# Kernel optimization log

Measured on AMD Instinct MI355X. Metric: run time of the kernel, lower is better.

## Reference

```python
import jax, jax.numpy as jnp
import numpy as np

B, S, H, DH = 2, 4096, 8, 64
D = H * DH


def setup_inputs() -> dict:
    key = jax.random.key(0)
    ks = jax.random.split(key, 6)
    std = 1.0 / np.sqrt(D)
    return {
        "x": jax.random.normal(ks[0], (B, S, D), dtype=jnp.float32),
        "Wq": jax.random.normal(ks[1], (D, D), dtype=jnp.float32) * std,
        "Wk": jax.random.normal(ks[2], (D, D), dtype=jnp.float32) * std,
        "Wv": jax.random.normal(ks[3], (D, D), dtype=jnp.float32) * std,
        "Wo": jax.random.normal(ks[4], (D, D), dtype=jnp.float32) * std,
        "bo": jnp.zeros((D,), dtype=jnp.float32),
    }


def reference(x, Wq, Wk, Wv, Wo, bo):
    scale = DH ** (-0.5)
    # torch Linear: y = x @ W.T
    q = x @ Wq.T  # [B,S,D]
    k = x @ Wk.T
    v = x @ Wv.T
    # split heads -> [B,H,S,Dh]
    q = q.reshape(B, S, H, DH).transpose(0, 2, 1, 3)
    k = k.reshape(B, S, H, DH).transpose(0, 2, 1, 3)
    v = v.reshape(B, S, H, DH).transpose(0, 2, 1, 3)
    score = jnp.einsum('bhqd,bhkd->bhqk', q, k) * scale  # [B,H,S,S]
    weights = jax.nn.softmax(score, axis=-1)
    attn = jnp.einsum('bhqk,bhkd->bhqd', weights, v)  # [B,H,S,Dh]
    h_ = attn.transpose(0, 2, 1, 3).reshape(B, S, D)
    return h_ @ Wo.T + bo
```

## Files before the change

kernel.cpp:

```cpp
#include <hip/hip_runtime.h>

#define LOG2E 1.44269504088896340736f

typedef unsigned short u16;
typedef __bf16 bf16x4_t __attribute__((ext_vector_type(4)));
typedef __bf16 bf16x8_t __attribute__((ext_vector_type(8)));
typedef float f32x4_t __attribute__((ext_vector_type(4)));

__device__ __forceinline__ f32x4_t mfma16(bf16x8_t a, bf16x8_t b, f32x4_t c) {
  return __builtin_amdgcn_mfma_f32_16x16x32_bf16(a, b, c, 0, 0, 0);
}

__device__ __forceinline__ void gl_lds16(const u16* g, u16* l) {
  __builtin_amdgcn_global_load_lds(
      (const __attribute__((address_space(1))) unsigned int*)g,
      (__attribute__((address_space(3))) unsigned int*)l, 16, 0, 0);
}

__device__ __forceinline__ void cvt_store(u16* dst, f32x4_t a, f32x4_t b, float scale) {
  a *= scale; b *= scale;
  union { uint4 u; struct { bf16x4_t lo, hi; } s; } c;
  c.s.lo = __builtin_convertvector(a, bf16x4_t);
  c.s.hi = __builtin_convertvector(b, bf16x4_t);
  *(uint4*)dst = c.u;
}

template <int MODE>
__device__ __forceinline__ void gemm_core_f32(const float* __restrict__ A, const float* __restrict__ Bt,
                                              u16* __restrict__ Cout, int Mbase, int Nbase,
                                              float bscale) {
  __shared__ __align__(16) u16 As[128][40];
  __shared__ __align__(16) u16 Bs[128][40];
  const int t = threadIdx.x;
  const int wave = t >> 6, lane = t & 63;
  const int r = lane & 15, qd = lane >> 4;
  const int wm = wave & 1, wn = wave >> 1;
  const int lr = t >> 2;
  const int lc = (t & 3) * 8;

  f32x4_t acc[4][4];
#pragma unroll
  for (int i = 0; i < 4; i++)
#pragma unroll
    for (int j = 0; j < 4; j++) { f32x4_t z = {0.f, 0.f, 0.f, 0.f}; acc[i][j] = z; }

  const float* pa0 = A  + (Mbase + lr) * 512 + lc;
  const float* pa1 = A  + (Mbase + 64 + lr) * 512 + lc;
  const float* pb0 = Bt + (Nbase + lr) * 512 + lc;
  const float* pb1 = Bt + (Nbase + 64 + lr) * 512 + lc;

  f32x4_t ra0[2], ra1[2], rb0[2], rb1[2];
  ra0[0] = *(const f32x4_t*)(pa0); ra0[1] = *(const f32x4_t*)(pa0 + 4);
  ra1[0] = *(const f32x4_t*)(pa1); ra1[1] = *(const f32x4_t*)(pa1 + 4);
  rb0[0] = *(const f32x4_t*)(pb0); rb0[1] = *(const f32x4_t*)(pb0 + 4);
  rb1[0] = *(const f32x4_t*)(pb1); rb1[1] = *(const f32x4_t*)(pb1 + 4);

  for (int k0 = 0; k0 < 512; k0 += 32) {
    cvt_store(&As[lr][lc],      ra0[0], ra0[1], 1.f);
    cvt_store(&As[64 + lr][lc], ra1[0], ra1[1], 1.f);
    cvt_store(&Bs[lr][lc],      rb0[0], rb0[1], bscale);
    cvt_store(&Bs[64 + lr][lc], rb1[0], rb1[1], bscale);
    __syncthreads();
    if (k0 < 480) {
      ra0[0] = *(const f32x4_t*)(pa0 + k0 + 32); ra0[1] = *(const f32x4_t*)(pa0 + k0 + 36);
      ra1[0] = *(const f32x4_t*)(pa1 + k0 + 32); ra1[1] = *(const f32x4_t*)(pa1 + k0 + 36);
      rb0[0] = *(const f32x4_t*)(pb0 + k0 + 32); rb0[1] = *(const f32x4_t*)(pb0 + k0 + 36);
      rb1[0] = *(const f32x4_t*)(pb1 + k0 + 32); rb1[1] = *(const f32x4_t*)(pb1 + k0 + 36);
    }
    bf16x8_t af[4], bfr[4];
#pragma unroll
    for (int i = 0; i < 4; i++) af[i]  = *(const bf16x8_t*)&As[wm * 64 + i * 16 + r][qd * 8];
#pragma unroll
    for (int j = 0; j < 4; j++) bfr[j] = *(const bf16x8_t*)&Bs[wn * 64 + j * 16 + r][qd * 8];
#pragma unroll
    for (int i = 0; i < 4; i++)
#pragma unroll
      for (int j = 0; j < 4; j++) acc[i][j] = mfma16(af[i], bfr[j], acc[i][j]);
    __syncthreads();
  }

#pragma unroll
  for (int i = 0; i < 4; i++) {
#pragma unroll
    for (int reg = 0; reg < 4; reg++) {
      int gr = Mbase + wm * 64 + i * 16 + qd * 4 + reg;
#pragma unroll
      for (int j = 0; j < 4; j++) {
        int gc = Nbase + wn * 64 + j * 16 + r;
        float val = acc[i][j][reg];
        if (MODE == 1) {
          int bb = gc >> 12, ss = gc & 4095;
          ((__bf16*)Cout)[((long)(bb * 512 + gr)) * 4096 + ss] = (__bf16)val;
        } else {
          ((__bf16*)Cout)[gr * 512 + gc] = (__bf16)val;
        }
      }
    }
  }
}

__global__ __launch_bounds__(256) void gemm_qkv_kernel(
    const float* __restrict__ X,
    const float* __restrict__ Wq, const float* __restrict__ Wk, const float* __restrict__ Wv,
    u16* __restrict__ Q, u16* __restrict__ K, u16* __restrict__ Vt) {
  if (blockIdx.z == 0)
    gemm_core_f32<0>(X, Wq, Q, blockIdx.x * 128, blockIdx.y * 128, 0.125f * LOG2E);
  else if (blockIdx.z == 1)
    gemm_core_f32<0>(X, Wk, K, blockIdx.x * 128, blockIdx.y * 128, 1.f);
  else
    gemm_core_f32<1>(Wv, X, Vt, blockIdx.y * 128, blockIdx.x * 128, 1.f);
}

__global__ __launch_bounds__(256) void gemm_out_kernel(
    const u16* __restrict__ Aat, const float* __restrict__ Wo,
    float* __restrict__ Out, const float* __restrict__ bo) {
  __shared__ __align__(16) u16 As[64][40];
  __shared__ __align__(16) u16 Bs[128][40];
  const int t = threadIdx.x;
  const int wave = t >> 6, lane = t & 63;
  const int r = lane & 15, qd = lane >> 4;
  const int wn = wave;
  const int Mbase = blockIdx.x * 64, Nbase = blockIdx.y * 128;
  const int lr = t >> 2;
  const int lc = (t & 3) * 8;

  f32x4_t acc[4][2];
#pragma unroll
  for (int i = 0; i < 4; i++)
#pragma unroll
    for (int j = 0; j < 2; j++) { f32x4_t z = {0.f, 0.f, 0.f, 0.f}; acc[i][j] = z; }

  const u16*  pa  = Aat + (Mbase + lr) * 512 + lc;
  const float* pb0 = Wo + (Nbase + lr) * 512 + lc;
  const float* pb1 = Wo + (Nbase + 64 + lr) * 512 + lc;

  uint4 ra = *(const uint4*)(pa);
  f32x4_t rb0[2], rb1[2];
  rb0[0] = *(const f32x4_t*)(pb0); rb0[1] = *(const f32x4_t*)(pb0 + 4);
  rb1[0] = *(const f32x4_t*)(pb1); rb1[1] = *(const f32x4_t*)(pb1 + 4);

  for (int k0 = 0; k0 < 512; k0 += 32) {
    *(uint4*)&As[lr][lc] = ra;
    cvt_store(&Bs[lr][lc],      rb0[0], rb0[1], 1.f);
    cvt_store(&Bs[64 + lr][lc], rb1[0], rb1[1], 1.f);
    __syncthreads();
    if (k0 < 480) {
      ra = *(const uint4*)(pa + k0 + 32);
      rb0[0] = *(const f32x4_t*)(pb0 + k0 + 32); rb0[1] = *(const f32x4_t*)(pb0 + k0 + 36);
      rb1[0] = *(const f32x4_t*)(pb1 + k0 + 32); rb1[1] = *(const f32x4_t*)(pb1 + k0 + 36);
    }
    bf16x8_t af[4], bfr[2];
#pragma unroll
    for (int i = 0; i < 4; i++) af[i]  = *(const bf16x8_t*)&As[i * 16 + r][qd * 8];
#pragma unroll
    for (int j = 0; j < 2; j++) bfr[j] = *(const bf16x8_t*)&Bs[wn * 32 + j * 16 + r][qd * 8];
#pragma unroll
    for (int i = 0; i < 4; i++)
#pragma unroll
      for (int j = 0; j < 2; j++) acc[i][j] = mfma16(af[i], bfr[j], acc[i][j]);
    __syncthreads();
  }

  float bv[2];
#pragma unroll
  for (int j = 0; j < 2; j++) bv[j] = bo[Nbase + wn * 32 + j * 16 + r];
#pragma unroll
  for (int i = 0; i < 4; i++)
#pragma unroll
    for (int reg = 0; reg < 4; reg++) {
      int gr = Mbase + i * 16 + qd * 4 + reg;
#pragma unroll
      for (int j = 0; j < 2; j++) {
        int gc = Nbase + wn * 32 + j * 16 + r;
        Out[gr * 512 + gc] = acc[i][j][reg] + bv[j];
      }
    }
}

__global__ __launch_bounds__(256, 2) void attn_kernel(
    const u16* __restrict__ Q, const u16* __restrict__ K, const u16* __restrict__ Vt,
    u16* __restrict__ Oattn) {
  __shared__ __align__(16) u16 Ks[2][2][4096];
  __shared__ __align__(16) u16 Vs[2][2][4096];

  const int t = threadIdx.x;
  const int wave = t >> 6, lane = t & 63;
  const int r = lane & 15, qd = lane >> 4;
  const int g = wave & 1, kv = wave >> 1;
  const int bh = blockIdx.y;
  const int b = bh >> 3, h = bh & 7;
  const long bbase = (long)b * 4096 * 512;
  const int q0 = blockIdx.x * 128;

  const int sw = r & 7;
  const int ck0 = (qd ^ sw) * 8;
  const int ck1 = ((qd + 4) ^ sw) * 8;
  int vo0[2], vo1[2];
#pragma unroll
  for (int c = 0; c < 2; c++) {
    vo0[c] = ((c * 4 + (qd >> 1)) ^ sw) * 8 + 4 * (qd & 1);
    vo1[c] = ((c * 4 + 2 + (qd >> 1)) ^ sw) * 8 + 4 * (qd & 1);
  }

  bf16x8_t ones8;
#pragma unroll
  for (int j = 0; j < 8; j++) ones8[j] = (__bf16)1.0f;

  bf16x8_t qf[4][2];
#pragma unroll
  for (int qa = 0; qa < 4; qa++) {
    const u16* qp = Q + bbase + (long)(q0 + g * 64 + qa * 16 + r) * 512 + h * 64 + qd * 8;
    qf[qa][0] = *(const bf16x8_t*)(qp);
    qf[qa][1] = *(const bf16x8_t*)(qp + 32);
  }

  f32x4_t accO[4][4];
  f32x4_t accL[4];
#pragma unroll
  for (int qa = 0; qa < 4; qa++) {
    f32x4_t z = {0.f, 0.f, 0.f, 0.f};
    accL[qa] = z;
#pragma unroll
    for (int nt = 0; nt < 4; nt++) accO[qa][nt] = z;
  }

  const int rr = lane >> 3;
  const int cc = (lane & 7) ^ rr;
  const u16* kgb = K + bbase + (long)(kv * 2048 + g * 32 + rr) * 512 + h * 64 + cc * 8;
  const u16* vgb = Vt + ((long)(b * 512 + h * 64 + g * 32 + rr)) * 4096 + kv * 2048 + cc * 8;

#pragma unroll
  for (int i = 0; i < 4; i++) gl_lds16(kgb + (long)i * 8 * 512, &Ks[kv][0][g * 2048] + i * 512);
#pragma unroll
  for (int i = 0; i < 4; i++) gl_lds16(vgb + i * 8 * 4096, &Vs[kv][0][g * 2048] + i * 512);

  for (int it = 0; it < 32; it++) {
    const int buf = it & 1;
    __syncthreads();

    if (it < 31) {
      const int nb = (it + 1) & 1;
      const long ko = (long)(it + 1) * 64;
#pragma unroll
      for (int i = 0; i < 4; i++)
        gl_lds16(kgb + (ko + i * 8) * 512, &Ks[kv][nb][g * 2048] + i * 512);
#pragma unroll
      for (int i = 0; i < 4; i++)
        gl_lds16(vgb + ko + (long)i * 8 * 4096, &Vs[kv][nb][g * 2048] + i * 512);
    }

    bf16x8_t kf[4][2];
#pragma unroll
    for (int nt = 0; nt < 4; nt++) {
      const u16* kb = &Ks[kv][buf][(nt * 16 + r) * 64];
      kf[nt][0] = *(const bf16x8_t*)(kb + ck0);
      kf[nt][1] = *(const bf16x8_t*)(kb + ck1);
    }

    f32x4_t St[4][4];
#pragma unroll
    for (int qa = 0; qa < 4; qa++)
#pragma unroll
      for (int nt = 0; nt < 4; nt++) {
        f32x4_t z = {0.f, 0.f, 0.f, 0.f};
        z = mfma16(kf[nt][0], qf[qa][0], z);
        z = mfma16(kf[nt][1], qf[qa][1], z);
        St[qa][nt] = z;
      }

    bf16x8_t pf[4][2];
#pragma unroll
    for (int qa = 0; qa < 4; qa++)
#pragma unroll
      for (int c = 0; c < 2; c++) {
        f32x4_t e0, e1;
#pragma unroll
        for (int j = 0; j < 4; j++) {
          e0[j] = __builtin_amdgcn_exp2f(St[qa][2 * c][j]);
          e1[j] = __builtin_amdgcn_exp2f(St[qa][2 * c + 1][j]);
        }
        bf16x4_t b0 = __builtin_convertvector(e0, bf16x4_t);
        bf16x4_t b1 = __builtin_convertvector(e1, bf16x4_t);
        bf16x8_t p8;
#pragma unroll
        for (int j = 0; j < 4; j++) { p8[j] = b0[j]; p8[4 + j] = b1[j]; }
        pf[qa][c] = p8;
      }

#pragma unroll
    for (int qa = 0; qa < 4; qa++)
#pragma unroll
      for (int c = 0; c < 2; c++)
        accL[qa] = mfma16(ones8, pf[qa][c], accL[qa]);

#pragma unroll
    for (int c = 0; c < 2; c++) {
      bf16x8_t va[4];
#pragma unroll
      for (int dm = 0; dm < 4; dm++) {
        const u16* vb = &Vs[kv][buf][(dm * 16 + r) * 64];
        union { uint4 u; bf16x8_t v; } cat;
        *(uint2*)&cat.u.x = *(const uint2*)(vb + vo0[c]);
        *(uint2*)&cat.u.z = *(const uint2*)(vb + vo1[c]);
        va[dm] = cat.v;
      }
#pragma unroll
      for (int qa = 0; qa < 4; qa++)
#pragma unroll
        for (int dm = 0; dm < 4; dm++)
          accO[qa][dm] = mfma16(va[dm], pf[qa][c], accO[qa][dm]);
    }
  }

  __syncthreads();
  float* Sc  = (float*)&Ks[0][0][0];
  float* Lsc = (float*)&Vs[0][0][0];
  if (kv == 1) {
#pragma unroll
    for (int qa = 0; qa < 4; qa++) {
#pragma unroll
      for (int dm = 0; dm < 4; dm++)
        *(f32x4_t*)&Sc[g * 4096 + ((qa * 4 + dm) * 64 + lane) * 4] = accO[qa][dm];
      Lsc[g * 256 + qa * 64 + lane] = accL[qa][0];
    }
  }
  __syncthreads();
  if (kv == 0) {
#pragma unroll
    for (int qa = 0; qa < 4; qa++) {
      float L = accL[qa][0] + Lsc[g * 256 + qa * 64 + lane];
      float inv = 1.f / L;
      int gq = q0 + g * 64 + qa * 16 + r;
#pragma unroll
      for (int dm = 0; dm < 4; dm++) {
        f32x4_t o = *(const f32x4_t*)&Sc[g * 4096 + ((qa * 4 + dm) * 64 + lane) * 4];
        o += accO[qa][dm];
        bf16x4_t ob;
#pragma unroll
        for (int reg = 0; reg < 4; reg++) ob[reg] = (__bf16)(o[reg] * inv);
        *(uint2*)&Oattn[bbase + (long)gq * 512 + h * 64 + dm * 16 + qd * 4] = *(uint2*)&ob;
      }
    }
  }
}

extern "C" void kernel_launch(void* const* d_in, const int* in_sizes, int n_in,
                              void* d_out, int out_size, void* d_ws, size_t ws_size,
                              hipStream_t stream) {
  const float* x  = (const float*)d_in[0];
  const float* Wq = (const float*)d_in[1];
  const float* Wk = (const float*)d_in[2];
  const float* Wv = (const float*)d_in[3];
  const float* Wo = (const float*)d_in[4];
  const float* bo = (const float*)d_in[5];
  float* out = (float*)d_out;

  u16* ws  = (u16*)d_ws;
  u16* Qb  = ws;
  u16* Kb  = Qb  + 4194304;
  u16* Vtg = Kb  + 4194304;
  u16* Ab  = Vtg + 4194304;

  dim3 g1(64, 4, 3);
  gemm_qkv_kernel<<<g1, 256, 0, stream>>>(x, Wq, Wk, Wv, Qb, Kb, Vtg);

  dim3 g2(32, 16);
  attn_kernel<<<g2, 256, 0, stream>>>(Qb, Kb, Vtg, Ab);

  dim3 g3(128, 4);
  gemm_out_kernel<<<g3, 256, 0, stream>>>(Ab, Wo, out, bo);
}
```

Before: 190.0 us.

## Pre-cast inputs to bf16 and use direct-to-LDS swizzled loads in GEMMs

Adds a separate cast kernel that converts x and all weights to bf16 once, with the Q scale folded into Wq. The projection GEMMs then stream bf16 through global_load_lds into an XOR-swizzled 64-wide LDS tile, and the output GEMM reuses the same 128x128 core. The aim is to halve GEMM read traffic and drop the per-tile fp32 convert and register staging. It also adds setprio around the MFMA blocks in attention. The costs are an extra kernel launch plus a full write and read of the bf16 copies, and the GEMM loop is no longer software-pipelined.

Result: no change. 186.7 us (-1.7%).

```diff
diff --git a/kernel.cpp b/kernel.cpp
--- a/kernel.cpp
+++ b/kernel.cpp
@@ -17,26 +17,42 @@
       (__attribute__((address_space(3))) unsigned int*)l, 16, 0, 0);
 }
 
-__device__ __forceinline__ void cvt_store(u16* dst, f32x4_t a, f32x4_t b, float scale) {
-  a *= scale; b *= scale;
+__global__ __launch_bounds__(256) void cast_kernel(
+    const float* __restrict__ x, const float* __restrict__ Wq, const float* __restrict__ Wk,
+    const float* __restrict__ Wv, const float* __restrict__ Wo,
+    u16* __restrict__ Xb, u16* __restrict__ Wqb, u16* __restrict__ Wkb,
+    u16* __restrict__ Wvb, u16* __restrict__ Wob) {
+  const int bid = blockIdx.x;
+  const float* src;
+  u16* dst;
+  float scale = 1.f;
+  int rel;
+  if (bid < 2048)      { src = x;  dst = Xb;  rel = bid; }
+  else if (bid < 2176) { src = Wq; dst = Wqb; rel = bid - 2048; scale = 0.125f * LOG2E; }
+  else if (bid < 2304) { src = Wk; dst = Wkb; rel = bid - 2176; }
+  else if (bid < 2432) { src = Wv; dst = Wvb; rel = bid - 2304; }
+  else                 { src = Wo; dst = Wob; rel = bid - 2432; }
+  const int i = rel * 2048 + threadIdx.x * 8;
+  f32x4_t a = *(const f32x4_t*)(src + i) * scale;
+  f32x4_t b = *(const f32x4_t*)(src + i + 4) * scale;
   union { uint4 u; struct { bf16x4_t lo, hi; } s; } c;
   c.s.lo = __builtin_convertvector(a, bf16x4_t);
   c.s.hi = __builtin_convertvector(b, bf16x4_t);
-  *(uint4*)dst = c.u;
+  *(uint4*)(dst + i) = c.u;
 }
 
 template <int MODE>
-__device__ __forceinline__ void gemm_core_f32(const float* __restrict__ A, const float* __restrict__ Bt,
-                                              u16* __restrict__ Cout, int Mbase, int Nbase,
-                                              float bscale) {
-  __shared__ __align__(16) u16 As[128][40];
-  __shared__ __align__(16) u16 Bs[128][40];
+__device__ __forceinline__ void gemm_core_bf16(const u16* __restrict__ A, const u16* __restrict__ Bt,
+                                               void* __restrict__ Cout, const float* __restrict__ bo,
+                                               int Mbase, int Nbase) {
+  __shared__ __align__(16) u16 As[128][64];
+  __shared__ __align__(16) u16 Bs[128][64];
   const int t = threadIdx.x;
   const int wave = t >> 6, lane = t & 63;
   const int r = lane & 15, qd = lane >> 4;
   const int wm = wave & 1, wn = wave >> 1;
-  const int lr = t >> 2;
-  const int lc = (t & 3) * 8;
+  const int rr = lane >> 3;
+  const int s8 = ((lane & 7) ^ (rr & 7)) * 8;
 
   f32x4_t acc[4][4];
 #pragma unroll
@@ -44,41 +60,39 @@
 #pragma unroll
     for (int j = 0; j < 4; j++) { f32x4_t z = {0.f, 0.f, 0.f, 0.f}; acc[i][j] = z; }
 
-  const float* pa0 = A  + (Mbase + lr) * 512 + lc;
-  const float* pa1 = A  + (Mbase + 64 + lr) * 512 + lc;
-  const float* pb0 = Bt + (Nbase + lr) * 512 + lc;
-  const float* pb1 = Bt + (Nbase + 64 + lr) * 512 + lc;
-
-  f32x4_t ra0[2], ra1[2], rb0[2], rb1[2];
-  ra0[0] = *(const f32x4_t*)(pa0); ra0[1] = *(const f32x4_t*)(pa0 + 4);
-  ra1[0] = *(const f32x4_t*)(pa1); ra1[1] = *(const f32x4_t*)(pa1 + 4);
-  rb0[0] = *(const f32x4_t*)(pb0); rb0[1] = *(const f32x4_t*)(pb0 + 4);
-  rb1[0] = *(const f32x4_t*)(pb1); rb1[1] = *(const f32x4_t*)(pb1 + 4);
-
-  for (int k0 = 0; k0 < 512; k0 += 32) {
-    cvt_store(&As[lr][lc],      ra0[0], ra0[1], 1.f);
-    cvt_store(&As[64 + lr][lc], ra1[0], ra1[1], 1.f);
-    cvt_store(&Bs[lr][lc],      rb0[0], rb0[1], bscale);
-    cvt_store(&Bs[64 + lr][lc], rb1[0], rb1[1], bscale);
+  const u16* pa = A  + (Mbase + wave * 32 + rr) * 512 + s8;
+  const u16* pb = Bt + (Nbase + wave * 32 + rr) * 512 + s8;
+  u16* la = &As[wave * 32][0];
+  u16* lb = &Bs[wave * 32][0];
+
+  for (int k0 = 0; k0 < 512; k0 += 64) {
+#pragma unroll
+    for (int j = 0; j < 4; j++) gl_lds16(pa + k0 + j * 8 * 512, la + j * 8 * 64);
+#pragma unroll
+    for (int j = 0; j < 4; j++) gl_lds16(pb + k0 + j * 8 * 512, lb + j * 8 * 64);
     __syncthreads();
-    if (k0 < 480) {
-      ra0[0] = *(const f32x4_t*)(pa0 + k0 + 32); ra0[1] = *(const f32x4_t*)(pa0 + k0 + 36);
-      ra1[0] = *(const f32x4_t*)(pa1 + k0 + 32); ra1[1] = *(const f32x4_t*)(pa1 + k0 + 36);
-      rb0[0] = *(const f32x4_t*)(pb0 + k0 + 32); rb0[1] = *(const f32x4_t*)(pb0 + k0 + 36);
-      rb1[0] = *(const f32x4_t*)(pb1 + k0 + 32); rb1[1] = *(const f32x4_t*)(pb1 + k0 + 36);
-    }
-    bf16x8_t af[4], bfr[4];
-#pragma unroll
-    for (int i = 0; i < 4; i++) af[i]  = *(const bf16x8_t*)&As[wm * 64 + i * 16 + r][qd * 8];
-#pragma unroll
-    for (int j = 0; j < 4; j++) bfr[j] = *(const bf16x8_t*)&Bs[wn * 64 + j * 16 + r][qd * 8];
-#pragma unroll
-    for (int i = 0; i < 4; i++)
-#pragma unroll
-      for (int j = 0; j < 4; j++) acc[i][j] = mfma16(af[i], bfr[j], acc[i][j]);
+#pragma unroll
+    for (int h = 0; h < 2; h++) {
+      bf16x8_t af[4], bfr[4];
+#pragma unroll
+      for (int i = 0; i < 4; i++)
+        af[i]  = *(const bf16x8_t*)&As[wm * 64 + i * 16 + r][((h * 4 + qd) ^ (r & 7)) * 8];
+#pragma unroll
+      for (int j = 0; j < 4; j++)
+        bfr[j] = *(const bf16x8_t*)&Bs[wn * 64 + j * 16 + r][((h * 4 + qd) ^ (r & 7)) * 8];
+#pragma unroll
+      for (int i = 0; i < 4; i++)
+#pragma unroll
+        for (int j = 0; j < 4; j++) acc[i][j] = mfma16(af[i], bfr[j], acc[i][j]);
+    }
     __syncthreads();
   }
 
+  float bv[4];
+  if (MODE == 2) {
+#pragma unroll
+    for (int j = 0; j < 4; j++) bv[j] = bo[Nbase + wn * 64 + j * 16 + r];
+  }
 #pragma unroll
   for (int i = 0; i < 4; i++) {
 #pragma unroll
@@ -91,8 +105,10 @@
         if (MODE == 1) {
           int bb = gc >> 12, ss = gc & 4095;
           ((__bf16*)Cout)[((long)(bb * 512 + gr)) * 4096 + ss] = (__bf16)val;
+        } else if (MODE == 0) {
+          ((__bf16*)Cout)[gr * 512 + gc] = (__bf16)val;
         } else {
-          ((__bf16*)Cout)[gr * 512 + gc] = (__bf16)val;
+          ((float*)Cout)[gr * 512 + gc] = val + bv[j];
         }
       }
     }
@@ -100,81 +116,21 @@
 }
 
 __global__ __launch_bounds__(256) void gemm_qkv_kernel(
-    const float* __restrict__ X,
-    const float* __restrict__ Wq, const float* __restrict__ Wk, const float* __restrict__ Wv,
+    const u16* __restrict__ Xb,
+    const u16* __restrict__ Wqb, const u16* __restrict__ Wkb, const u16* __restrict__ Wvb,
     u16* __restrict__ Q, u16* __restrict__ K, u16* __restrict__ Vt) {
   if (blockIdx.z == 0)
-    gemm_core_f32<0>(X, Wq, Q, blockIdx.x * 128, blockIdx.y * 128, 0.125f * LOG2E);
+    gemm_core_bf16<0>(Xb, Wqb, Q, nullptr, blockIdx.x * 128, blockIdx.y * 128);
   else if (blockIdx.z == 1)
-    gemm_core_f32<0>(X, Wk, K, blockIdx.x * 128, blockIdx.y * 128, 1.f);
+    gemm_core_bf16<0>(Xb, Wkb, K, nullptr, blockIdx.x * 128, blockIdx.y * 128);
   else
-    gemm_core_f32<1>(Wv, X, Vt, blockIdx.y * 128, blockIdx.x * 128, 1.f);
+    gemm_core_bf16<1>(Wvb, Xb, Vt, nullptr, blockIdx.y * 128, blockIdx.x * 128);
 }
 
 __global__ __launch_bounds__(256) void gemm_out_kernel(
-    const u16* __restrict__ Aat, const float* __restrict__ Wo,
+    const u16* __restrict__ Aat, const u16* __restrict__ Wob,
     float* __restrict__ Out, const float* __restrict__ bo) {
-  __shared__ __align__(16) u16 As[64][40];
-  __shared__ __align__(16) u16 Bs[128][40];
-  const int t = threadIdx.x;
-  const int wave = t >> 6, lane = t & 63;
-  const int r = lane & 15, qd = lane >> 4;
-  const int wn = wave;
-  const int Mbase = blockIdx.x * 64, Nbase = blockIdx.y * 128;
-  const int lr = t >> 2;
-  const int lc = (t & 3) * 8;
-
-  f32x4_t acc[4][2];
-#pragma unroll
-  for (int i = 0; i < 4; i++)
-#pragma unroll
-    for (int j = 0; j < 2; j++) { f32x4_t z = {0.f, 0.f, 0.f, 0.f}; acc[i][j] = z; }
-
-  const u16*  pa  = Aat + (Mbase + lr) * 512 + lc;
-  const float* pb0 = Wo + (Nbase + lr) * 512 + lc;
-  const float* pb1 = Wo + (Nbase + 64 + lr) * 512 + lc;
-
-  uint4 ra = *(const uint4*)(pa);
-  f32x4_t rb0[2], rb1[2];
-  rb0[0] = *(const f32x4_t*)(pb0); rb0[1] = *(const f32x4_t*)(pb0 + 4);
-  rb1[0] = *(const f32x4_t*)(pb1); rb1[1] = *(const f32x4_t*)(pb1 + 4);
-
-  for (int k0 = 0; k0 < 512; k0 += 32) {
-    *(uint4*)&As[lr][lc] = ra;
-    cvt_store(&Bs[lr][lc],      rb0[0], rb0[1], 1.f);
-    cvt_store(&Bs[64 + lr][lc], rb1[0], rb1[1], 1.f);
-    __syncthreads();
-    if (k0 < 480) {
-      ra = *(const uint4*)(pa + k0 + 32);
-      rb0[0] = *(const f32x4_t*)(pb0 + k0 + 32); rb0[1] = *(const f32x4_t*)(pb0 + k0 + 36);
-      rb1[0] = *(const f32x4_t*)(pb1 + k0 + 32); rb1[1] = *(const f32x4_t*)(pb1 + k0 + 36);
-    }
-    bf16x8_t af[4], bfr[2];
-#pragma unroll
-    for (int i = 0; i < 4; i++) af[i]  = *(const bf16x8_t*)&As[i * 16 + r][qd * 8];
-#pragma unroll
-    for (int j = 0; j < 2; j++) bfr[j] = *(const bf16x8_t*)&Bs[wn * 32 + j * 16 + r][qd * 8];
-#pragma unroll
-    for (int i = 0; i < 4; i++)
-#pragma unroll
-      for (int j = 0; j < 2; j++) acc[i][j] = mfma16(af[i], bfr[j], acc[i][j]);
-    __syncthreads();
-  }
-
-  float bv[2];
-#pragma unroll
-  for (int j = 0; j < 2; j++) bv[j] = bo[Nbase + wn * 32 + j * 16 + r];
-#pragma unroll
-  for (int i = 0; i < 4; i++)
-#pragma unroll
-    for (int reg = 0; reg < 4; reg++) {
-      int gr = Mbase + i * 16 + qd * 4 + reg;
-#pragma unroll
-      for (int j = 0; j < 2; j++) {
-        int gc = Nbase + wn * 32 + j * 16 + r;
-        Out[gr * 512 + gc] = acc[i][j][reg] + bv[j];
-      }
-    }
+  gemm_core_bf16<2>(Aat, Wob, Out, bo, blockIdx.x * 128, blockIdx.y * 128);
 }
 
 __global__ __launch_bounds__(256, 2) void attn_kernel(
@@ -258,6 +214,7 @@
     }
 
     f32x4_t St[4][4];
+    __builtin_amdgcn_s_setprio(1);
 #pragma unroll
     for (int qa = 0; qa < 4; qa++)
 #pragma unroll
@@ -267,6 +224,7 @@
         z = mfma16(kf[nt][1], qf[qa][1], z);
         St[qa][nt] = z;
       }
+    __builtin_amdgcn_s_setprio(0);
 
     bf16x8_t pf[4][2];
 #pragma unroll
@@ -304,11 +262,13 @@
         *(uint2*)&cat.u.z = *(const uint2*)(vb + vo1[c]);
         va[dm] = cat.v;
       }
+      __builtin_amdgcn_s_setprio(1);
 #pragma unroll
       for (int qa = 0; qa < 4; qa++)
 #pragma unroll
         for (int dm = 0; dm < 4; dm++)
           accO[qa][dm] = mfma16(va[dm], pf[qa][c], accO[qa][dm]);
+      __builtin_amdgcn_s_setprio(0);
     }
   }
 
@@ -360,13 +320,20 @@
   u16* Kb  = Qb  + 4194304;
   u16* Vtg = Kb  + 4194304;
   u16* Ab  = Vtg + 4194304;
+  u16* Xb  = Ab;
+  u16* Wqb = Ab  + 4194304;
+  u16* Wkb = Wqb + 262144;
+  u16* Wvb = Wkb + 262144;
+  u16* Wob = Wvb + 262144;
+
+  cast_kernel<<<2560, 256, 0, stream>>>(x, Wq, Wk, Wv, Wo, Xb, Wqb, Wkb, Wvb, Wob);
 
   dim3 g1(64, 4, 3);
-  gemm_qkv_kernel<<<g1, 256, 0, stream>>>(x, Wq, Wk, Wv, Qb, Kb, Vtg);
+  gemm_qkv_kernel<<<g1, 256, 0, stream>>>(Xb, Wqb, Wkb, Wvb, Qb, Kb, Vtg);
 
   dim3 g2(32, 16);
   attn_kernel<<<g2, 256, 0, stream>>>(Qb, Kb, Vtg, Ab);
 
-  dim3 g3(128, 4);
-  gemm_out_kernel<<<g3, 256, 0, stream>>>(Ab, Wo, out, bo);
-}
+  dim3 g3(64, 4);
+  gemm_out_kernel<<<g3, 256, 0, stream>>>(Ab, Wob, out, bo);
+}
```
